# Kernel tuning notes

Hardware: AMD Instinct MI355X
Metric: run time of the kernel (lower is better)

Reference implementation:

```python
import jax, jax.numpy as jnp
import numpy as np

B, D, H, W, T = 16, 64, 160, 320, 20

def setup_inputs() -> dict:
    key = jax.random.key(0)
    k1, k2 = jax.random.split(key)
    x1 = jax.random.normal(k1, (B, D, H, W), dtype=jnp.float32)
    x2 = jax.random.normal(k2, (1, T, D), dtype=jnp.float32)
    x2_mask = jnp.ones((1, T), dtype=jnp.int32)
    return {"x1": x1, "x2": x2, "x2_mask": x2_mask}

def reference(x1, x2, x2_mask):
    # x1: [B, D, H, W]; x2: [1, T, D]; x2_mask: [1, T]
    b, d, h, w = x1.shape
    x1_flat = x1.reshape(b, d, h * w)                       # [B, D, N]
    tokens = x2[0]                                          # [T, D] (same token broadcast over batch, as in .repeat(B,1))
    # raw_score = x1_flat^T @ token  -> [B, T, N]; softmax over spatial dim N
    scores = jnp.einsum('bdn,td->btn', x1_flat, tokens)
    attn = jax.nn.softmax(scores, axis=2)                   # [B, T, N]
    m = x2_mask[0].astype(x1.dtype)                         # [T], masked-sum over valid tokens
    count = jnp.sum(m)
    weight = jnp.einsum('btn,t->bn', attn, m) / count       # [B, N]: (1/x2_len) * sum_t attn_t
    out = x1_flat * weight[:, None, :]                      # [B, D, N]
    return out.reshape(b, d, h, w)
```

## Files before the change

kernel.cpp:

```cpp
#include <hip/hip_runtime.h>
#include <math.h>

#define BDIM 16
#define DDIM 64
#define TDIM 20
#define NDIM (160*320)

constexpr int K1_THREADS = 256;
constexpr int K1_NPT     = 4;
constexpr int K1_CHUNK   = K1_THREADS * K1_NPT;
constexpr int K1_NB      = NDIM / K1_CHUNK;

__global__ __launch_bounds__(K1_THREADS)
void k_stats(const float* __restrict__ x1,
             const float* __restrict__ tok,
             float* __restrict__ pstats)
{
    const int b   = blockIdx.y;
    const int nb  = blockIdx.x;
    const int tid = threadIdx.x;
    const int n0  = nb * K1_CHUNK + tid * 4;
    const float* xb = x1 + (size_t)b * DDIM * NDIM + n0;

    float acc[TDIM][4];
#pragma unroll
    for (int t = 0; t < TDIM; ++t)
        acc[t][0] = acc[t][1] = acc[t][2] = acc[t][3] = 0.f;

#pragma unroll 4
    for (int d = 0; d < DDIM; ++d) {
        const float4 v = *(const float4*)(xb + (size_t)d * NDIM);
#pragma unroll
        for (int t = 0; t < TDIM; ++t) {
            const float tk = tok[t * DDIM + d];
            acc[t][0] = fmaf(v.x, tk, acc[t][0]);
            acc[t][1] = fmaf(v.y, tk, acc[t][1]);
            acc[t][2] = fmaf(v.z, tk, acc[t][2]);
            acc[t][3] = fmaf(v.w, tk, acc[t][3]);
        }
    }

    float m[TDIM], s[TDIM];
#pragma unroll
    for (int t = 0; t < TDIM; ++t) {
        const float mm = fmaxf(fmaxf(acc[t][0], acc[t][1]),
                               fmaxf(acc[t][2], acc[t][3]));
        m[t] = mm;
        s[t] = __expf(acc[t][0] - mm) + __expf(acc[t][1] - mm) +
               __expf(acc[t][2] - mm) + __expf(acc[t][3] - mm);
    }

#pragma unroll
    for (int t = 0; t < TDIM; ++t) {
        float mm = m[t], ss = s[t];
        for (int off = 32; off; off >>= 1) {
            const float m2 = __shfl_xor(mm, off);
            const float s2 = __shfl_xor(ss, off);
            const float mx = fmaxf(mm, m2);
            ss = ss * __expf(mm - mx) + s2 * __expf(m2 - mx);
            mm = mx;
        }
        m[t] = mm; s[t] = ss;
    }

    __shared__ float red[4][TDIM][2];
    const int wave = tid >> 6;
    const int lane = tid & 63;
    if (lane == 0) {
#pragma unroll
        for (int t = 0; t < TDIM; ++t) {
            red[wave][t][0] = m[t];
            red[wave][t][1] = s[t];
        }
    }
    __syncthreads();
    if (tid < TDIM) {
        float mm = red[0][tid][0], ss = red[0][tid][1];
#pragma unroll
        for (int w = 1; w < 4; ++w) {
            const float m2 = red[w][tid][0], s2 = red[w][tid][1];
            const float mx = fmaxf(mm, m2);
            ss = ss * __expf(mm - mx) + s2 * __expf(m2 - mx);
            mm = mx;
        }
        float* o = pstats + ((size_t)(nb * BDIM + b) * TDIM + tid) * 2;
        o[0] = mm;
        o[1] = ss;
    }
}

__global__ void k_merge(const float* __restrict__ pstats,
                        const int* __restrict__ mask,
                        float* __restrict__ stats)
{
    const int i = threadIdx.x;
    if (i >= BDIM * TDIM) return;
    const int b = i / TDIM;
    const int t = i % TDIM;

    float mm = -INFINITY, ss = 0.f;
    for (int nb = 0; nb < K1_NB; ++nb) {
        const float* p = pstats + ((size_t)(nb * BDIM + b) * TDIM + t) * 2;
        const float m2 = p[0], s2 = p[1];
        const float mx = fmaxf(mm, m2);
        ss = ss * __expf(mm - mx) + s2 * __expf(m2 - mx);
        mm = mx;
    }
    float cnt = 0.f;
#pragma unroll
    for (int tt = 0; tt < TDIM; ++tt) cnt += (float)mask[tt];
    const float c = (float)mask[t] / (ss * cnt);
    stats[(b * TDIM + t) * 2 + 0] = mm;
    stats[(b * TDIM + t) * 2 + 1] = c;
}

__global__ __launch_bounds__(256)
void k_out(const float* __restrict__ x1,
           const float* __restrict__ tok,
           const float* __restrict__ stats,
           float* __restrict__ out)
{
    const int b = blockIdx.y;
    const int n = blockIdx.x * 256 + threadIdx.x;
    const size_t base = (size_t)b * DDIM * NDIM + n;

    float v[DDIM];
#pragma unroll
    for (int d = 0; d < DDIM; ++d)
        v[d] = x1[base + (size_t)d * NDIM];

    float acc[TDIM];
#pragma unroll
    for (int t = 0; t < TDIM; ++t) acc[t] = 0.f;

#pragma unroll 8
    for (int d = 0; d < DDIM; ++d) {
        const float vd = v[d];
#pragma unroll
        for (int t = 0; t < TDIM; ++t)
            acc[t] = fmaf(vd, tok[t * DDIM + d], acc[t]);
    }

    float w = 0.f;
#pragma unroll
    for (int t = 0; t < TDIM; ++t) {
        const float M = stats[(b * TDIM + t) * 2 + 0];
        const float C = stats[(b * TDIM + t) * 2 + 1];
        w = fmaf(__expf(acc[t] - M), C, w);
    }

#pragma unroll
    for (int d = 0; d < DDIM; ++d)
        out[base + (size_t)d * NDIM] = v[d] * w;
}

extern "C" void kernel_launch(void* const* d_in, const int* in_sizes, int n_in,
                              void* d_out, int out_size, void* d_ws, size_t ws_size,
                              hipStream_t stream)
{
    const float* x1   = (const float*)d_in[0];
    const float* x2   = (const float*)d_in[1];
    const int*   mask = (const int*)d_in[2];
    float* out = (float*)d_out;

    float* pstats = (float*)d_ws;
    float* stats  = pstats + (size_t)K1_NB * BDIM * TDIM * 2;

    k_stats<<<dim3(K1_NB, BDIM), K1_THREADS, 0, stream>>>(x1, x2, pstats);
    k_merge<<<1, 320, 0, stream>>>(pstats, mask, stats);
    k_out<<<dim3(NDIM / 256, BDIM), 256, 0, stream>>>(x1, x2, stats, out);
}
```

Measured before the change: 489.5 us.

## Vectorize output kernel with float4 and parallelize softmax stats merge across blocks

The output kernel now has each thread handle four spatial positions, using float4 loads for the score pass and a second float4 re-read of x1 for the scaled write, instead of holding 64 scalar values in registers. This is meant to cut register pressure and use wider memory transactions, at the cost of reading x1 twice per thread (the second read may hit in cache). The merge kernel moves from one block with a serial loop over partial stats to a grid of (batch, token) blocks that combine the 50 partials with a wave shuffle reduction, removing a long serial tail. The -INFINITY start value is swapped for a large finite negative so empty lanes do not produce NaNs in the exp combine.

```diff
diff --git a/kernel.cpp b/kernel.cpp
--- a/kernel.cpp
+++ b/kernel.cpp
@@ -5,6 +5,8 @@
 #define DDIM 64
 #define TDIM 20
 #define NDIM (160*320)
+
+#define NEG_HUGE (-3.402823466e38f)
 
 constexpr int K1_THREADS = 256;
 constexpr int K1_NPT     = 4;
@@ -89,29 +91,36 @@
     }
 }
 
-__global__ void k_merge(const float* __restrict__ pstats,
-                        const int* __restrict__ mask,
-                        float* __restrict__ stats)
+__global__ __launch_bounds__(64)
+void k_merge(const float* __restrict__ pstats,
+             const int* __restrict__ mask,
+             float* __restrict__ stats)
 {
-    const int i = threadIdx.x;
-    if (i >= BDIM * TDIM) return;
-    const int b = i / TDIM;
-    const int t = i % TDIM;
+    const int b = blockIdx.x;
+    const int t = blockIdx.y;
+    const int l = threadIdx.x;
 
-    float mm = -INFINITY, ss = 0.f;
-    for (int nb = 0; nb < K1_NB; ++nb) {
-        const float* p = pstats + ((size_t)(nb * BDIM + b) * TDIM + t) * 2;
-        const float m2 = p[0], s2 = p[1];
+    float mm = NEG_HUGE, ss = 0.f;
+    if (l < K1_NB) {
+        const float* p = pstats + ((size_t)(l * BDIM + b) * TDIM + t) * 2;
+        mm = p[0];
+        ss = p[1];
+    }
+    for (int off = 32; off; off >>= 1) {
+        const float m2 = __shfl_xor(mm, off);
+        const float s2 = __shfl_xor(ss, off);
         const float mx = fmaxf(mm, m2);
         ss = ss * __expf(mm - mx) + s2 * __expf(m2 - mx);
         mm = mx;
     }
-    float cnt = 0.f;
+    if (l == 0) {
+        float cnt = 0.f;
 #pragma unroll
-    for (int tt = 0; tt < TDIM; ++tt) cnt += (float)mask[tt];
-    const float c = (float)mask[t] / (ss * cnt);
-    stats[(b * TDIM + t) * 2 + 0] = mm;
-    stats[(b * TDIM + t) * 2 + 1] = c;
+        for (int tt = 0; tt < TDIM; ++tt) cnt += (float)mask[tt];
+        const float c = (float)mask[t] / (ss * cnt);
+        stats[(b * TDIM + t) * 2 + 0] = mm;
+        stats[(b * TDIM + t) * 2 + 1] = c;
+    }
 }
 
 __global__ __launch_bounds__(256)
@@ -120,38 +129,47 @@
            const float* __restrict__ stats,
            float* __restrict__ out)
 {
-    const int b = blockIdx.y;
-    const int n = blockIdx.x * 256 + threadIdx.x;
-    const size_t base = (size_t)b * DDIM * NDIM + n;
+    const int b  = blockIdx.y;
+    const int n0 = (blockIdx.x * 256 + threadIdx.x) * 4;
+    const size_t base = (size_t)b * DDIM * NDIM + n0;
 
-    float v[DDIM];
+    float acc[TDIM][4];
 #pragma unroll
-    for (int d = 0; d < DDIM; ++d)
-        v[d] = x1[base + (size_t)d * NDIM];
+    for (int t = 0; t < TDIM; ++t)
+        acc[t][0] = acc[t][1] = acc[t][2] = acc[t][3] = 0.f;
 
-    float acc[TDIM];
+#pragma unroll 4
+    for (int d = 0; d < DDIM; ++d) {
+        const float4 v = *(const float4*)(x1 + base + (size_t)d * NDIM);
 #pragma unroll
-    for (int t = 0; t < TDIM; ++t) acc[t] = 0.f;
-
-#pragma unroll 8
-    for (int d = 0; d < DDIM; ++d) {
-        const float vd = v[d];
-#pragma unroll
-        for (int t = 0; t < TDIM; ++t)
-            acc[t] = fmaf(vd, tok[t * DDIM + d], acc[t]);
+        for (int t = 0; t < TDIM; ++t) {
+            const float tk = tok[t * DDIM + d];
+            acc[t][0] = fmaf(v.x, tk, acc[t][0]);
+            acc[t][1] = fmaf(v.y, tk, acc[t][1]);
+            acc[t][2] = fmaf(v.z, tk, acc[t][2]);
+            acc[t][3] = fmaf(v.w, tk, acc[t][3]);
+        }
     }
 
-    float w = 0.f;
+    float w0 = 0.f, w1 = 0.f, w2 = 0.f, w3 = 0.f;
 #pragma unroll
     for (int t = 0; t < TDIM; ++t) {
         const float M = stats[(b * TDIM + t) * 2 + 0];
         const float C = stats[(b * TDIM + t) * 2 + 1];
-        w = fmaf(__expf(acc[t] - M), C, w);
+        w0 = fmaf(__expf(acc[t][0] - M), C, w0);
+        w1 = fmaf(__expf(acc[t][1] - M), C, w1);
+        w2 = fmaf(__expf(acc[t][2] - M), C, w2);
+        w3 = fmaf(__expf(acc[t][3] - M), C, w3);
     }
 
-#pragma unroll
-    for (int d = 0; d < DDIM; ++d)
-        out[base + (size_t)d * NDIM] = v[d] * w;
+    __asm__ __volatile__("" ::: "memory");
+
+#pragma unroll 4
+    for (int d = 0; d < DDIM; ++d) {
+        float4 v = *(const float4*)(x1 + base + (size_t)d * NDIM);
+        v.x *= w0; v.y *= w1; v.z *= w2; v.w *= w3;
+        *(float4*)(out + base + (size_t)d * NDIM) = v;
+    }
 }
 
 extern "C" void kernel_launch(void* const* d_in, const int* in_sizes, int n_in,
@@ -167,6 +185,6 @@
     float* stats  = pstats + (size_t)K1_NB * BDIM * TDIM * 2;
 
     k_stats<<<dim3(K1_NB, BDIM), K1_THREADS, 0, stream>>>(x1, x2, pstats);
-    k_merge<<<1, 320, 0, stream>>>(pstats, mask, stats);
-    k_out<<<dim3(NDIM / 256, BDIM), 256, 0, stream>>>(x1, x2, stats, out);
+    k_merge<<<dim3(BDIM, TDIM), 64, 0, stream>>>(pstats, mask, stats);
+    k_out<<<dim3(NDIM / 1024, BDIM), 256, 0, stream>>>(x1, x2, stats, out);
 }
```

New measurement: 488.1 us. No clear change (-0.3%).
